# Performance work log

Hardware: AMD Instinct MI355X
Metric: run time of the kernel (lower is better)

Reference implementation:

```python
import jax, jax.numpy as jnp
import numpy as np

B, S, H, NH, HD = 2, 2048, 2048, 16, 128
E, TOPK, I = 8, 2, 2048
EPS = 1e-5
ROPE_THETA = 10000.0


def setup_inputs() -> dict:
    key = jax.random.key(0)
    ks = jax.random.split(key, 11)
    s = 0.02
    return {
        "hidden_states": jax.random.normal(ks[0], (B, S, H), jnp.float32),
        "position_ids": jnp.broadcast_to(jnp.arange(S, dtype=jnp.int32), (B, S)),
        "rms1_w": jnp.ones((H,), jnp.float32),
        "rms2_w": jnp.ones((H,), jnp.float32),
        "q_w": jax.random.normal(ks[1], (H, H), jnp.float32) * s,
        "k_w": jax.random.normal(ks[2], (H, H), jnp.float32) * s,
        "v_w": jax.random.normal(ks[3], (H, H), jnp.float32) * s,
        "o_w": jax.random.normal(ks[4], (H, H), jnp.float32) * s,
        "router_w": jax.random.normal(ks[5], (H, E), jnp.float32) * s,
        "w1": jax.random.normal(ks[6], (E, H, I), jnp.float32) * s,
        "w2": jax.random.normal(ks[7], (E, I, H), jnp.float32) * s,
        "w3": jax.random.normal(ks[8], (E, H, I), jnp.float32) * s,
    }


def rmsnorm(x, w):
    var = jnp.mean(x * x, axis=-1, keepdims=True)
    return (x * jax.lax.rsqrt(var + EPS)) * w


def rope(x, pos):
    # x: [B,S,NH,HD], pos: [B,S]
    half = HD // 2
    inv_freq = 1.0 / (ROPE_THETA ** (jnp.arange(0, half, dtype=jnp.float32) / half))
    ang = pos.astype(jnp.float32)[..., None] * inv_freq  # [B,S,half]
    cos = jnp.cos(ang)[:, :, None, :]
    sin = jnp.sin(ang)[:, :, None, :]
    x1, x2 = x[..., :half], x[..., half:]
    return jnp.concatenate([x1 * cos - x2 * sin, x2 * cos + x1 * sin], axis=-1)


def attention(x, pos, q_w, k_w, v_w, o_w):
    q = (x @ q_w).reshape(B, S, NH, HD)
    k = (x @ k_w).reshape(B, S, NH, HD)
    v = (x @ v_w).reshape(B, S, NH, HD)
    q = rope(q, pos)
    k = rope(k, pos)
    scores = jnp.einsum("bqhd,bkhd->bhqk", q, k) / np.sqrt(HD).astype(np.float32)
    causal = jnp.tril(jnp.ones((S, S), bool))
    scores = jnp.where(causal, scores, jnp.finfo(scores.dtype).min)
    probs = jax.nn.softmax(scores, axis=-1)
    ctx = jnp.einsum("bhqk,bkhd->bqhd", probs, v).reshape(B, S, H)
    return ctx @ o_w


def moe(x, router_w, w1, w2, w3):
    t = x.reshape(B * S, H)
    probs = jax.nn.softmax(t @ router_w, axis=-1)  # [T,E]
    top_v, top_i = jax.lax.top_k(probs, TOPK)
    top_v = top_v / jnp.sum(top_v, axis=-1, keepdims=True)
    T = B * S
    coeff = jnp.zeros((T, E), x.dtype).at[jnp.arange(T)[:, None], top_i].set(top_v)
    y = jnp.zeros((T, H), x.dtype)
    for e in range(E):  # fixed small expert loop
        h = jax.nn.silu(t @ w1[e]) * (t @ w3[e])
        y = y + coeff[:, e:e + 1] * (h @ w2[e])
    return y.reshape(B, S, H)


def reference(hidden_states, position_ids, rms1_w, rms2_w, q_w, k_w, v_w, o_w,
              router_w, w1, w2, w3):
    residual = hidden_states
    h = rmsnorm(hidden_states, rms1_w).astype(hidden_states.dtype)
    h = attention(h, position_ids, q_w, k_w, v_w, o_w)
    h = residual + h
    residual = h
    h = rmsnorm(h, rms2_w).astype(h.dtype)
    h = moe(h, router_w, w1, w2, w3)
    return residual + h
```

## Files before the change

kernel.cpp:

```cpp
#include <hip/hip_runtime.h>
#include <hip/hip_bf16.h>

constexpr int CB   = 2;
constexpr int CS   = 2048;
constexpr int CH   = 2048;
constexpr int CNH  = 16;
constexpr int CHD  = 128;
constexpr int CE   = 8;
constexpr int CI   = 2048;
constexpr int CT   = CB * CS;
constexpr int CQKV = 3 * CH;

typedef __attribute__((ext_vector_type(8))) short short8;
typedef __attribute__((ext_vector_type(4))) float float4v;
typedef __attribute__((ext_vector_type(4))) unsigned short ushort4v;
typedef unsigned int uint32;

__device__ __forceinline__ float bf2f(unsigned short u) {
    union { unsigned int i; float f; } x; x.i = ((unsigned int)u) << 16; return x.f;
}
__device__ __forceinline__ unsigned short f2bf(float f) {
    union { float f; unsigned int i; } x; x.f = f;
    unsigned int r = x.i + 0x7fffu + ((x.i >> 16) & 1u);
    return (unsigned short)(r >> 16);
}
__device__ __forceinline__ uint32 packpair(uint32 r0, uint32 r1) {
    return __builtin_amdgcn_perm(r1, r0, 0x07060302u);
}
__device__ __forceinline__ uint32 rnebits(float f) {
    uint32 u = __float_as_uint(f);
    return u + 0x7fffu + ((u >> 16) & 1u);
}
__device__ __forceinline__ void split2(float f0, float f1, uint32& h, uint32& l) {
    uint32 r0 = rnebits(f0), r1 = rnebits(f1);
    h = packpair(r0, r1);
    float d0 = f0 - __uint_as_float(r0 & 0xffff0000u);
    float d1 = f1 - __uint_as_float(r1 & 0xffff0000u);
    l = packpair(rnebits(d0), rnebits(d1));
}
__device__ __forceinline__ void rne16_store(const float* fv, unsigned short* dst) {
    uint32 h[8];
    #pragma unroll
    for (int p = 0; p < 8; p++) h[p] = packpair(rnebits(fv[2 * p]), rnebits(fv[2 * p + 1]));
    ((uint4*)dst)[0] = make_uint4(h[0], h[1], h[2], h[3]);
    ((uint4*)dst)[1] = make_uint4(h[4], h[5], h[6], h[7]);
}

template<int MODE>
__global__ __launch_bounds__(256) void rmsnorm_k(const float* __restrict__ x,
                                                 const float* __restrict__ w,
                                                 unsigned short* __restrict__ o1,
                                                 unsigned short* __restrict__ o2) {
    const int row = blockIdx.x;
    const float* xr = x + (size_t)row * CH;
    const int base = threadIdx.x * 8;
    float4 v0 = *(const float4*)(xr + base);
    float4 v1 = *(const float4*)(xr + base + 4);
    float ss = v0.x*v0.x + v0.y*v0.y + v0.z*v0.z + v0.w*v0.w
             + v1.x*v1.x + v1.y*v1.y + v1.z*v1.z + v1.w*v1.w;
    #pragma unroll
    for (int o = 1; o < 64; o <<= 1) ss += __shfl_xor(ss, o);
    __shared__ float ps[4];
    if ((threadIdx.x & 63) == 0) ps[threadIdx.x >> 6] = ss;
    __syncthreads();
    const float scale = rsqrtf((ps[0] + ps[1] + ps[2] + ps[3]) / (float)CH + 1e-5f);
    float4 w0 = *(const float4*)(w + base);
    float4 w1 = *(const float4*)(w + base + 4);
    float r[8] = {v0.x * scale * w0.x, v0.y * scale * w0.y, v0.z * scale * w0.z, v0.w * scale * w0.w,
                  v1.x * scale * w1.x, v1.y * scale * w1.y, v1.z * scale * w1.z, v1.w * scale * w1.w};
    if (MODE == 1) {
        rne16_store(r, o1 + (size_t)row * CH + base);
    } else {
        uint32 h[4], l[4];
        #pragma unroll
        for (int p = 0; p < 4; p++) split2(r[2 * p], r[2 * p + 1], h[p], l[p]);
        *(uint4*)(o1 + (size_t)row * CH + base) = make_uint4(h[0], h[1], h[2], h[3]);
        *(uint4*)(o2 + (size_t)row * CH + base) = make_uint4(l[0], l[1], l[2], l[3]);
    }
}

__global__ void rope_tab_k(float2* __restrict__ tab) {
    int i = blockIdx.x * 256 + threadIdx.x;
    int p = i >> 6, j = i & 63;
    double inv = pow(10000.0, -(double)j / 64.0);
    float invf = (float)inv;
    float angf = (float)p * invf;
    double da = (double)angf;
    tab[i] = make_float2((float)cos(da), (float)sin(da));
}

__global__ __launch_bounds__(256) void rope_k(unsigned short* __restrict__ qh,
                                              unsigned short* __restrict__ ql,
                                              const int* __restrict__ pos,
                                              const float2* __restrict__ tab) {
    int i = blockIdx.x * 256 + threadIdx.x;
    if (i >= CT * CNH * 64) return;
    int t = i >> 10, hj = i & 1023, hh = hj >> 6, j = hj & 63;
    float2 cs = tab[(size_t)pos[t] * 64 + j];
    unsigned short* qhp = qh + (size_t)t * CQKV + hh * CHD;
    unsigned short* qlp = ql + (size_t)t * CQKV + hh * CHD;
    #pragma unroll
    for (int s = 0; s < 2; s++) {
        unsigned short* hp = qhp + s * CH;
        unsigned short* lp = qlp + s * CH;
        float x1 = bf2f(hp[j]) + bf2f(lp[j]);
        float x2 = bf2f(hp[j + 64]) + bf2f(lp[j + 64]);
        float y1 = x1 * cs.x - x2 * cs.y;
        float y2 = x2 * cs.x + x1 * cs.y;
        uint32 r1 = rnebits(y1), r2 = rnebits(y2);
        hp[j]      = (unsigned short)(r1 >> 16);
        hp[j + 64] = (unsigned short)(r2 >> 16);
        lp[j]      = f2bf(y1 - __uint_as_float(r1 & 0xffff0000u));
        lp[j + 64] = f2bf(y2 - __uint_as_float(r2 & 0xffff0000u));
    }
}

template<int NMAT>
__global__ __launch_bounds__(256) void conv_k(const float* __restrict__ S0,
                                              const float* __restrict__ S1,
                                              unsigned short* __restrict__ D) {
    __shared__ float t[64][65];
    const int n0 = blockIdx.x * 64, k0 = blockIdx.y * 64, e = blockIdx.z;
    const size_t esrc = (size_t)e * 2048 * 2048;
    const int cc = threadIdx.x & 63, r4 = threadIdx.x >> 6;
    const int nl = threadIdx.x >> 2, q = threadIdx.x & 3;
    #pragma unroll
    for (int s = 0; s < NMAT; s++) {
        const float* S = s ? S1 : S0;
        __syncthreads();
        #pragma unroll
        for (int j = 0; j < 16; j++) {
            const int row = j * 4 + r4;
            t[cc][row] = S[esrc + (size_t)(k0 + row) * 2048 + n0 + cc];
        }
        __syncthreads();
        const int orow = (NMAT == 2) ? (2 * (n0 + nl) + s) : (n0 + nl);
        unsigned short* dp = D + (size_t)e * (NMAT * 2048) * 2048 + (size_t)orow * 2048 + k0 + q * 16;
        float fv[16];
        #pragma unroll
        for (int j = 0; j < 16; j++) fv[j] = t[nl][q * 16 + j];
        rne16_store(fv, dp);
    }
}

template<int NMAT>
__global__ __launch_bounds__(256) void convs_k(const float* __restrict__ S0,
                                               const float* __restrict__ S1,
                                               const float* __restrict__ S2,
                                               unsigned short* __restrict__ Dh,
                                               unsigned short* __restrict__ Dl) {
    __shared__ float t[64][65];
    const int n0 = blockIdx.x * 64, k0 = blockIdx.y * 64, z = blockIdx.z;
    const float* S = S0;
    if (NMAT == 3) S = (z == 0) ? S0 : ((z == 1) ? S1 : S2);
    const int cc = threadIdx.x & 63, r4 = threadIdx.x >> 6;
    #pragma unroll
    for (int j = 0; j < 16; j++) {
        const int row = j * 4 + r4;
        t[cc][row] = S[(size_t)(k0 + row) * 2048 + n0 + cc];
    }
    __syncthreads();
    const int nl = threadIdx.x >> 2, q = threadIdx.x & 3;
    float fv[16];
    #pragma unroll
    for (int j = 0; j < 16; j++) fv[j] = t[nl][q * 16 + j];
    uint32 h[8], l[8];
    #pragma unroll
    for (int p = 0; p < 8; p++) split2(fv[2 * p], fv[2 * p + 1], h[p], l[p]);
    const size_t off = (size_t)(z * 2048 + n0 + nl) * 2048 + k0 + q * 16;
    ((uint4*)(Dh + off))[0] = make_uint4(h[0], h[1], h[2], h[3]);
    ((uint4*)(Dh + off))[1] = make_uint4(h[4], h[5], h[6], h[7]);
    ((uint4*)(Dl + off))[0] = make_uint4(l[0], l[1], l[2], l[3]);
    ((uint4*)(Dl + off))[1] = make_uint4(l[4], l[5], l[6], l[7]);
}

template<int MODE>
__global__ __launch_bounds__(256) void sgemm_k(
    const unsigned short* __restrict__ Ahg, const unsigned short* __restrict__ Alg, int lda,
    const unsigned short* __restrict__ Bhg, const unsigned short* __restrict__ Blg, int K,
    unsigned short* __restrict__ Ch, unsigned short* __restrict__ Cl,
    float* __restrict__ Cf, int ldc,
    const float* __restrict__ resid, float* __restrict__ C2) {
    __shared__ unsigned short AhS[128][40], AlS[128][40], BhS[128][40], BlS[128][40];
    const int mt = blockIdx.x, nt = blockIdx.y, tid = threadIdx.x;
    const int m0 = mt * 128;
    const int srow = tid >> 1, shalf = tid & 1;
    const unsigned short* ah = Ahg + (size_t)(m0 + srow) * lda + shalf * 16;
    const unsigned short* al = Alg + (size_t)(m0 + srow) * lda + shalf * 16;
    const unsigned short* bhp = Bhg + (size_t)(nt * 128 + srow) * K + shalf * 16;
    const unsigned short* blp = Blg + (size_t)(nt * 128 + srow) * K + shalf * 16;
    const int lane = tid & 63, lr = lane & 15, lg = lane >> 4;
    const int wr = (tid >> 7) & 1, wc = (tid >> 6) & 1;

    float4v acc[4][4];
    #pragma unroll
    for (int m = 0; m < 4; m++)
        #pragma unroll
        for (int n = 0; n < 4; n++) acc[m][n] = (float4v){0.f, 0.f, 0.f, 0.f};

    short8 rah0 = *(const short8*)(ah),     rah1 = *(const short8*)(ah + 8);
    short8 ral0 = *(const short8*)(al),     ral1 = *(const short8*)(al + 8);
    short8 rbh0 = *(const short8*)(bhp),    rbh1 = *(const short8*)(bhp + 8);
    short8 rbl0 = *(const short8*)(blp),    rbl1 = *(const short8*)(blp + 8);

    for (int k0 = 0; k0 < K; k0 += 32) {
        __syncthreads();
        *(short8*)(&AhS[srow][shalf * 16])     = rah0;
        *(short8*)(&AhS[srow][shalf * 16 + 8]) = rah1;
        *(short8*)(&AlS[srow][shalf * 16])     = ral0;
        *(short8*)(&AlS[srow][shalf * 16 + 8]) = ral1;
        *(short8*)(&BhS[srow][shalf * 16])     = rbh0;
        *(short8*)(&BhS[srow][shalf * 16 + 8]) = rbh1;
        *(short8*)(&BlS[srow][shalf * 16])     = rbl0;
        *(short8*)(&BlS[srow][shalf * 16 + 8]) = rbl1;
        if (k0 + 32 < K) {
            rah0 = *(const short8*)(ah + k0 + 32);  rah1 = *(const short8*)(ah + k0 + 40);
            ral0 = *(const short8*)(al + k0 + 32);  ral1 = *(const short8*)(al + k0 + 40);
            rbh0 = *(const short8*)(bhp + k0 + 32); rbh1 = *(const short8*)(bhp + k0 + 40);
            rbl0 = *(const short8*)(blp + k0 + 32); rbl1 = *(const short8*)(blp + k0 + 40);
        }
        __syncthreads();
        short8 fah[4], fal[4], fbh[4], fbl[4];
        #pragma unroll
        for (int m = 0; m < 4; m++) {
            fah[m] = *(const short8*)(&AhS[wr * 64 + m * 16 + lr][lg * 8]);
            fal[m] = *(const short8*)(&AlS[wr * 64 + m * 16 + lr][lg * 8]);
        }
        #pragma unroll
        for (int n = 0; n < 4; n++) {
            fbh[n] = *(const short8*)(&BhS[wc * 64 + n * 16 + lr][lg * 8]);
            fbl[n] = *(const short8*)(&BlS[wc * 64 + n * 16 + lr][lg * 8]);
        }
        #pragma unroll
        for (int n = 0; n < 4; n++)
            #pragma unroll
            for (int m = 0; m < 4; m++) {
                acc[m][n] = __builtin_amdgcn_mfma_f32_16x16x32_bf16(fal[m], fbh[n], acc[m][n], 0, 0, 0);
                acc[m][n] = __builtin_amdgcn_mfma_f32_16x16x32_bf16(fah[m], fbl[n], acc[m][n], 0, 0, 0);
                acc[m][n] = __builtin_amdgcn_mfma_f32_16x16x32_bf16(fah[m], fbh[n], acc[m][n], 0, 0, 0);
            }
    }
    #pragma unroll
    for (int m = 0; m < 4; m++) {
        const int rb = wr * 64 + m * 16 + lg * 4;
        #pragma unroll
        for (int n = 0; n < 4; n++) {
            const int ccol = nt * 128 + wc * 64 + n * 16 + lr;
            #pragma unroll
            for (int r = 0; r < 4; r++) {
                const size_t idx = (size_t)(m0 + rb + r) * ldc + ccol;
                if (MODE == 1) {
                    const float v = acc[m][n][r] + resid[idx];
                    Cf[idx] = v;
                    C2[idx] = v;
                } else {
                    const float v = acc[m][n][r];
                    uint32 rr = rnebits(v);
                    Ch[idx] = (unsigned short)(rr >> 16);
                    Cl[idx] = f2bf(v - __uint_as_float(rr & 0xffff0000u));
                }
            }
        }
    }
}

template<int MODE>
__global__ __launch_bounds__(256) void gemm_k(
    const unsigned short* __restrict__ A, int lda,
    const unsigned short* __restrict__ Bt, int K, int Ne,
    void* __restrict__ Cp, int ldc,
    const int* __restrict__ cnt, const int* __restrict__ tokl,
    const float* __restrict__ gatel, const int* __restrict__ pb) {
    __shared__ unsigned short As[128][40];
    __shared__ unsigned short Bs[128][40];
    const int nt = blockIdx.x, mt = blockIdx.y, e = blockIdx.z;
    const int m0 = mt * 128;
    const int c = cnt[e];
    if (m0 >= c) return;
    const int valid = (c - m0 < 128) ? (c - m0) : 128;
    const int tid = threadIdx.x;
    const int srow = tid >> 1, shalf = tid & 1;
    size_t gr;
    if (MODE == 2) {
        const int idx = m0 + (srow < valid ? srow : valid - 1);
        gr = (size_t)tokl[e * 4096 + idx];
    } else {
        const int rr = m0 + srow;
        gr = (size_t)(pb[e] + (rr < c ? rr : c - 1));
    }
    const unsigned short* a_src = A + gr * (size_t)lda + shalf * 16;
    const unsigned short* b_src = Bt + (size_t)e * Ne * K + (size_t)(nt * 128 + srow) * K + shalf * 16;
    const int lane = tid & 63, lr = lane & 15, lg = lane >> 4;
    const int wr = (tid >> 7) & 1, wc = (tid >> 6) & 1;

    float4v acc[4][4];
    #pragma unroll
    for (int m = 0; m < 4; m++)
        #pragma unroll
        for (int n = 0; n < 4; n++) acc[m][n] = (float4v){0.f, 0.f, 0.f, 0.f};

    short8 ra0 = *(const short8*)(a_src);
    short8 ra1 = *(const short8*)(a_src + 8);
    short8 rb0 = *(const short8*)(b_src);
    short8 rb1 = *(const short8*)(b_src + 8);

    for (int k0 = 0; k0 < K; k0 += 32) {
        __syncthreads();
        *(short8*)(&As[srow][shalf * 16])     = ra0;
        *(short8*)(&As[srow][shalf * 16 + 8]) = ra1;
        *(short8*)(&Bs[srow][shalf * 16])     = rb0;
        *(short8*)(&Bs[srow][shalf * 16 + 8]) = rb1;
        if (k0 + 32 < K) {
            ra0 = *(const short8*)(a_src + k0 + 32);
            ra1 = *(const short8*)(a_src + k0 + 40);
            rb0 = *(const short8*)(b_src + k0 + 32);
            rb1 = *(const short8*)(b_src + k0 + 40);
        }
        __syncthreads();
        short8 af[4], bf[4];
        #pragma unroll
        for (int m = 0; m < 4; m++) af[m] = *(const short8*)(&As[wr * 64 + m * 16 + lr][lg * 8]);
        #pragma unroll
        for (int n = 0; n < 4; n++) bf[n] = *(const short8*)(&Bs[wc * 64 + n * 16 + lr][lg * 8]);
        #pragma unroll
        for (int n = 0; n < 4; n++)
            #pragma unroll
            for (int m = 0; m < 4; m++)
                acc[m][n] = __builtin_amdgcn_mfma_f32_16x16x32_bf16(af[m], bf[n], acc[m][n], 0, 0, 0);
    }

    #pragma unroll
    for (int m = 0; m < 4; m++) {
        const int rb = wr * 64 + m * 16 + lg * 4;
        #pragma unroll
        for (int n = 0; n < 4; n++) {
            const int col = nt * 128 + wc * 64 + n * 16 + lr;
            #pragma unroll
            for (int r = 0; r < 4; r++) {
                const int row = rb + r;
                const float v = acc[m][n][r];
                if (MODE == 2) {
                    const float other = __shfl_xor(v, 1);
                    if (!(lr & 1) && row < valid) {
                        const float g1 = v, g3 = other;
                        const float hsw = (g1 / (1.f + __expf(-g1))) * g3;
                        ((unsigned short*)Cp)[(size_t)(pb[e] + m0 + row) * ldc + (col >> 1)] = f2bf(hsw);
                    }
                } else {
                    if (row < valid) {
                        const int t = tokl[e * 4096 + m0 + row];
                        const float g = gatel[e * 4096 + m0 + row];
                        atomicAdd(((float*)Cp) + (size_t)t * ldc + col, v * g);
                    }
                }
            }
        }
    }
}

__global__ __launch_bounds__(256) void attn_k(const unsigned short* __restrict__ qh,
                                              const unsigned short* __restrict__ ql,
                                              unsigned short* __restrict__ ch,
                                              unsigned short* __restrict__ cl) {
    __shared__ unsigned short Ksh[32][136], Ksl[32][136];
    __shared__ unsigned short Vth[128][40], Vtl[128][40];
    const int qb = blockIdx.x;
    const int h  = blockIdx.y;
    const int b  = blockIdx.z;
    const int tid = threadIdx.x;
    const int wave = tid >> 6, lane = tid & 63, lr = lane & 15, lg = lane >> 4;
    const size_t tb = (size_t)b * CS;
    const int q0 = qb * 64 + wave * 16;

    short8 qfh[4], qfl[4];
    {
        const size_t off = (tb + q0 + lr) * CQKV + h * CHD;
        #pragma unroll
        for (int c = 0; c < 4; c++) {
            qfh[c] = *(const short8*)(qh + off + c * 32 + lg * 8);
            qfl[c] = *(const short8*)(ql + off + c * 32 + lg * 8);
        }
    }
    float4v o[8];
    #pragma unroll
    for (int d = 0; d < 8; d++) o[d] = (float4v){0.f, 0.f, 0.f, 0.f};
    float m = -1e30f, l = 0.f;
    const float scl = 0.08838834764831845f;
    const int ntiles = (qb * 64 + 64 + 31) >> 5;
    const int kk = tid >> 3, slot = tid & 7;
    const int vd = tid & 127, vhalf = tid >> 7;

    for (int kt = 0; kt < ntiles; ++kt) {
        const int kv0 = kt * 32;
        __syncthreads();
        {
            const size_t koff = (tb + kv0 + kk) * CQKV + CH + h * CHD + slot * 16;
            *(short8*)(&Ksh[kk][slot * 16])     = *(const short8*)(qh + koff);
            *(short8*)(&Ksh[kk][slot * 16 + 8]) = *(const short8*)(qh + koff + 8);
            *(short8*)(&Ksl[kk][slot * 16])     = *(const short8*)(ql + koff);
            *(short8*)(&Ksl[kk][slot * 16 + 8]) = *(const short8*)(ql + koff + 8);
            const size_t voff = (tb + kv0 + vhalf * 16) * CQKV + 2 * CH + h * CHD + vd;
            unsigned short th[16], tl[16];
            #pragma unroll
            for (int j = 0; j < 16; j++) {
                th[j] = qh[voff + (size_t)j * CQKV];
                tl[j] = ql[voff + (size_t)j * CQKV];
            }
            #pragma unroll
            for (int p = 0; p < 2; p++) {
                *(ushort4v*)(&Vth[vd][vhalf * 16 + p * 8])     = *(ushort4v*)(&th[p * 8]);
                *(ushort4v*)(&Vth[vd][vhalf * 16 + p * 8 + 4]) = *(ushort4v*)(&th[p * 8 + 4]);
                *(ushort4v*)(&Vtl[vd][vhalf * 16 + p * 8])     = *(ushort4v*)(&tl[p * 8]);
                *(ushort4v*)(&Vtl[vd][vhalf * 16 + p * 8 + 4]) = *(ushort4v*)(&tl[p * 8 + 4]);
            }
        }
        __syncthreads();

        float4v st0 = (float4v){0.f,0.f,0.f,0.f}, st1 = st0;
        #pragma unroll
        for (int c = 0; c < 4; c++) {
            short8 kah = *(const short8*)(&Ksh[lr][c * 32 + lg * 8]);
            short8 kal = *(const short8*)(&Ksl[lr][c * 32 + lg * 8]);
            short8 kbh = *(const short8*)(&Ksh[16 + lr][c * 32 + lg * 8]);
            short8 kbl = *(const short8*)(&Ksl[16 + lr][c * 32 + lg * 8]);
            st0 = __builtin_amdgcn_mfma_f32_16x16x32_bf16(kal, qfh[c], st0, 0, 0, 0);
            st0 = __builtin_amdgcn_mfma_f32_16x16x32_bf16(kah, qfl[c], st0, 0, 0, 0);
            st0 = __builtin_amdgcn_mfma_f32_16x16x32_bf16(kah, qfh[c], st0, 0, 0, 0);
            st1 = __builtin_amdgcn_mfma_f32_16x16x32_bf16(kbl, qfh[c], st1, 0, 0, 0);
            st1 = __builtin_amdgcn_mfma_f32_16x16x32_bf16(kbh, qfl[c], st1, 0, 0, 0);
            st1 = __builtin_amdgcn_mfma_f32_16x16x32_bf16(kbh, qfh[c], st1, 0, 0, 0);
        }
        float pv[8]; float pmax = -1e30f;
        const int qg = q0 + lr;
        #pragma unroll
        for (int f = 0; f < 2; f++) {
            #pragma unroll
            for (int r = 0; r < 4; r++) {
                const int kg = kv0 + f * 16 + lg * 4 + r;
                const float s = (kg <= qg) ? ((f ? st1[r] : st0[r]) * scl) : -1e30f;
                pv[f * 4 + r] = s;
                pmax = fmaxf(pmax, s);
            }
        }
        pmax = fmaxf(pmax, __shfl_xor(pmax, 16));
        pmax = fmaxf(pmax, __shfl_xor(pmax, 32));
        const float mnew = fmaxf(m, pmax);
        const float alpha = __expf(m - mnew);
        float sum = 0.f;
        #pragma unroll
        for (int i = 0; i < 8; i++) { const float p = __expf(pv[i] - mnew); pv[i] = p; sum += p; }
        sum += __shfl_xor(sum, 16);
        sum += __shfl_xor(sum, 32);
        l = l * alpha + sum;
        m = mnew;
        #pragma unroll
        for (int d = 0; d < 8; d++) o[d] *= alpha;
        short8 pfh, pfl;
        unsigned short* pfhp = (unsigned short*)&pfh;
        unsigned short* pflp = (unsigned short*)&pfl;
        #pragma unroll
        for (int j = 0; j < 8; j++) {
            const int srcl = (((lg & 1) * 2 + (j >> 2)) << 4) | lr;
            const float a0 = __shfl(pv[j & 3], srcl);
            const float a1 = __shfl(pv[4 + (j & 3)], srcl);
            const float sel = (lg >= 2) ? a1 : a0;
            uint32 r = rnebits(sel);
            pfhp[j] = (unsigned short)(r >> 16);
            float d = sel - __uint_as_float(r & 0xffff0000u);
            pflp[j] = (unsigned short)(rnebits(d) >> 16);
        }
        #pragma unroll
        for (int dt = 0; dt < 8; dt++) {
            short8 vh = *(const short8*)(&Vth[dt * 16 + lr][lg * 8]);
            short8 vl = *(const short8*)(&Vtl[dt * 16 + lr][lg * 8]);
            o[dt] = __builtin_amdgcn_mfma_f32_16x16x32_bf16(vl, pfh, o[dt], 0, 0, 0);
            o[dt] = __builtin_amdgcn_mfma_f32_16x16x32_bf16(vh, pfl, o[dt], 0, 0, 0);
            o[dt] = __builtin_amdgcn_mfma_f32_16x16x32_bf16(vh, pfh, o[dt], 0, 0, 0);
        }
    }
    const float inv = 1.f / l;
    const size_t coff = (tb + q0 + lr) * CH + h * CHD + lg * 4;
    #pragma unroll
    for (int dt = 0; dt < 8; dt++) {
        ushort4v wh, wl;
        #pragma unroll
        for (int r = 0; r < 4; r++) {
            const float v = o[dt][r] * inv;
            uint32 rr = rnebits(v);
            wh[r] = (unsigned short)(rr >> 16);
            wl[r] = f2bf(v - __uint_as_float(rr & 0xffff0000u));
        }
        *(ushort4v*)(ch + coff + dt * 16) = wh;
        *(ushort4v*)(cl + coff + dt * 16) = wl;
    }
}

__global__ __launch_bounds__(64) void router_k(const float* __restrict__ x,
                                               const float* __restrict__ wn,
                                               const float* __restrict__ rw,
                                               int* __restrict__ cnt, int* __restrict__ tok,
                                               float* __restrict__ gate) {
    const int t = blockIdx.x;
    const int lane = threadIdx.x;
    const float* xr = x + (size_t)t * CH;
    double ss = 0.0;
    double acc[8] = {0,0,0,0,0,0,0,0};
    for (int i = lane * 4; i < CH; i += 256) {
        float4 v = *(const float4*)(xr + i);
        float4 wv = *(const float4*)(wn + i);
        ss += (double)v.x*v.x + (double)v.y*v.y + (double)v.z*v.z + (double)v.w*v.w;
        float xs[4] = {v.x, v.y, v.z, v.w};
        float ws4[4] = {wv.x, wv.y, wv.z, wv.w};
        #pragma unroll
        for (int dd = 0; dd < 4; dd++) {
            const double xn = (double)xs[dd] * (double)ws4[dd];
            const float* rr = rw + (size_t)(i + dd) * CE;
            #pragma unroll
            for (int e2 = 0; e2 < 8; e2++) acc[e2] += xn * (double)rr[e2];
        }
    }
    #pragma unroll
    for (int o = 1; o < 64; o <<= 1) ss += __shfl_xor(ss, o);
    #pragma unroll
    for (int e2 = 0; e2 < 8; e2++) {
        #pragma unroll
        for (int o = 1; o < 64; o <<= 1) acc[e2] += __shfl_xor(acc[e2], o);
    }
    if (lane == 0) {
        const double scale = rsqrt(ss / (double)CH + 1e-5);
        int e0 = 0;
        #pragma unroll
        for (int e2 = 1; e2 < 8; e2++) if (acc[e2] > acc[e0]) e0 = e2;
        int e1 = (e0 == 0) ? 1 : 0;
        #pragma unroll
        for (int e2 = 0; e2 < 8; e2++) if (e2 != e0 && acc[e2] > acc[e1]) e1 = e2;
        const double dl = scale * (acc[e1] - acc[e0]);
        const double p1r = exp(dl);
        const float g0 = (float)(1.0 / (1.0 + p1r));
        const float g1 = (float)(p1r / (1.0 + p1r));
        int pos0 = atomicAdd(&cnt[e0], 1);
        tok[e0 * 4096 + pos0] = t; gate[e0 * 4096 + pos0] = g0;
        int pos1 = atomicAdd(&cnt[e1], 1);
        tok[e1 * 4096 + pos1] = t; gate[e1 * 4096 + pos1] = g1;
    }
}

__global__ void prefix_k(const int* __restrict__ cnt, int* __restrict__ pb) {
    if (threadIdx.x == 0 && blockIdx.x == 0) {
        int s = 0;
        for (int e = 0; e < CE; e++) { pb[e] = s; s += cnt[e]; }
    }
}

extern "C" void kernel_launch(void* const* d_in, const int* in_sizes, int n_in,
                              void* d_out, int out_size, void* d_ws, size_t ws_size,
                              hipStream_t stream) {
    (void)in_sizes; (void)n_in; (void)out_size; (void)ws_size;
    const float* hidden = (const float*)d_in[0];
    const int*   posids = (const int*)d_in[1];
    const float* rms1w  = (const float*)d_in[2];
    const float* rms2w  = (const float*)d_in[3];
    const float* qw     = (const float*)d_in[4];
    const float* kw     = (const float*)d_in[5];
    const float* vw     = (const float*)d_in[6];
    const float* ow     = (const float*)d_in[7];
    const float* rw     = (const float*)d_in[8];
    const float* w1     = (const float*)d_in[9];
    const float* w2     = (const float*)d_in[10];
    const float* w3     = (const float*)d_in[11];
    float* out = (float*)d_out;

    char* ws = (char*)d_ws;
    unsigned short* h1h = (unsigned short*)ws;
    unsigned short* h1l = (unsigned short*)(ws + 16777216);
    unsigned short* woh = (unsigned short*)ws;
    unsigned short* wol = (unsigned short*)(ws + 8388608);
    unsigned short* h2  = (unsigned short*)ws;
    int*   tok  = (int*)(ws + 16777216);
    float* gate = (float*)(ws + 16777216 + 131072);
    int*   cnt  = (int*)(ws + 16777216 + 262144);
    int*   pb   = cnt + 16;
    unsigned short* qkvh = (unsigned short*)(ws + 33554432);
    unsigned short* qkvl = (unsigned short*)(ws + 83886080);
    unsigned short* wt13 = (unsigned short*)(ws + 33554432);
    unsigned short* wt2  = (unsigned short*)(ws + 33554432);
    unsigned short* wqkvh = (unsigned short*)(ws + 134217728);
    unsigned short* wqkvl = (unsigned short*)(ws + 134217728 + 25165824);
    unsigned short* ctxh = (unsigned short*)(ws + 134217728);
    unsigned short* ctxl = (unsigned short*)(ws + 150994944);
    float*          res2 = (float*)(ws + 167772160);
    unsigned short* Hbuf = (unsigned short*)(ws + 167772160);
    float2*         rtab = (float2*)(ws + 201326592);

    rope_tab_k<<<512, 256, 0, stream>>>(rtab);
    rmsnorm_k<0><<<CT, 256, 0, stream>>>(hidden, rms1w, h1h, h1l);
    convs_k<3><<<dim3(32, 32, 3), 256, 0, stream>>>(qw, kw, vw, wqkvh, wqkvl);
    sgemm_k<0><<<dim3(32, 48), 256, 0, stream>>>(h1h, h1l, CH, wqkvh, wqkvl, CH,
                                                 qkvh, qkvl, nullptr, CQKV, nullptr, nullptr);
    rope_k<<<16384, 256, 0, stream>>>(qkvh, qkvl, posids, rtab);
    convs_k<1><<<dim3(32, 32, 1), 256, 0, stream>>>(ow, nullptr, nullptr, woh, wol);
    attn_k<<<dim3(32, CNH, CB), 256, 0, stream>>>(qkvh, qkvl, ctxh, ctxl);
    sgemm_k<1><<<dim3(32, 16), 256, 0, stream>>>(ctxh, ctxl, CH, woh, wol, CH,
                                                 nullptr, nullptr, res2, CH, hidden, out);
    rmsnorm_k<1><<<CT, 256, 0, stream>>>(res2, rms2w, h2, nullptr);
    hipMemsetAsync(cnt, 0, 8 * sizeof(int), stream);
    router_k<<<CT, 64, 0, stream>>>(res2, rms2w, rw, cnt, tok, gate);
    prefix_k<<<1, 64, 0, stream>>>(cnt, pb);
    conv_k<2><<<dim3(32, 32, CE), 256, 0, stream>>>(w1, w3, wt13);
    gemm_k<2><<<dim3(32, 32, CE), 256, 0, stream>>>(h2, CH, wt13, CH, 2 * CI, Hbuf, CI,
                                                    cnt, tok, gate, pb);
    conv_k<1><<<dim3(32, 32, CE), 256, 0, stream>>>(w2, nullptr, wt2);
    gemm_k<3><<<dim3(16, 32, CE), 256, 0, stream>>>(Hbuf, CI, wt2, CI, CH, out, CH,
                                                    cnt, tok, gate, pb);
}
```

Baseline: 1.523 ms.

## Prefetch next K/V tile into registers and remap attention blocks for XCD locality

```diff
diff --git a/kernel.cpp b/kernel.cpp
--- a/kernel.cpp
+++ b/kernel.cpp
@@ -364,9 +364,11 @@
                                               unsigned short* __restrict__ cl) {
     __shared__ unsigned short Ksh[32][136], Ksl[32][136];
     __shared__ unsigned short Vth[128][40], Vtl[128][40];
-    const int qb = blockIdx.x;
-    const int h  = blockIdx.y;
-    const int b  = blockIdx.z;
+    const int bid = blockIdx.x;
+    const int xcd = bid & 7, jj = bid >> 3;
+    const int bh  = xcd * 4 + (jj >> 5);
+    const int qb  = 31 - (jj & 31);
+    const int h   = bh & 15, b = bh >> 4;
     const int tid = threadIdx.x;
     const int wave = tid >> 6, lane = tid & 63, lr = lane & 15, lg = lane >> 4;
     const size_t tb = (size_t)b * CS;
@@ -386,32 +388,52 @@
     for (int d = 0; d < 8; d++) o[d] = (float4v){0.f, 0.f, 0.f, 0.f};
     float m = -1e30f, l = 0.f;
     const float scl = 0.08838834764831845f;
-    const int ntiles = (qb * 64 + 64 + 31) >> 5;
+    const int ntiles = 2 * (qb + 1);
     const int kk = tid >> 3, slot = tid & 7;
     const int vd = tid & 127, vhalf = tid >> 7;
 
+    short8 pkh0, pkh1, pkl0, pkl1;
+    unsigned short pth[16], ptl[16];
+    {
+        const size_t koff = (tb + kk) * CQKV + CH + h * CHD + slot * 16;
+        pkh0 = *(const short8*)(qh + koff);
+        pkh1 = *(const short8*)(qh + koff + 8);
+        pkl0 = *(const short8*)(ql + koff);
+        pkl1 = *(const short8*)(ql + koff + 8);
+        const size_t voff = (tb + vhalf * 16) * CQKV + 2 * CH + h * CHD + vd;
+        #pragma unroll
+        for (int j = 0; j < 16; j++) {
+            pth[j] = qh[voff + (size_t)j * CQKV];
+            ptl[j] = ql[voff + (size_t)j * CQKV];
+        }
+    }
+
     for (int kt = 0; kt < ntiles; ++kt) {
         const int kv0 = kt * 32;
         __syncthreads();
-        {
-            const size_t koff = (tb + kv0 + kk) * CQKV + CH + h * CHD + slot * 16;
-            *(short8*)(&Ksh[kk][slot * 16])     = *(const short8*)(qh + koff);
-            *(short8*)(&Ksh[kk][slot * 16 + 8]) = *(const short8*)(qh + koff + 8);
-            *(short8*)(&Ksl[kk][slot * 16])     = *(const short8*)(ql + koff);
-            *(short8*)(&Ksl[kk][slot * 16 + 8]) = *(const short8*)(ql + koff + 8);
-            const size_t voff = (tb + kv0 + vhalf * 16) * CQKV + 2 * CH + h * CHD + vd;
-            unsigned short th[16], tl[16];
+        *(short8*)(&Ksh[kk][slot * 16])     = pkh0;
+        *(short8*)(&Ksh[kk][slot * 16 + 8]) = pkh1;
+        *(short8*)(&Ksl[kk][slot * 16])     = pkl0;
+        *(short8*)(&Ksl[kk][slot * 16 + 8]) = pkl1;
+        #pragma unroll
+        for (int p = 0; p < 2; p++) {
+            *(ushort4v*)(&Vth[vd][vhalf * 16 + p * 8])     = *(ushort4v*)(&pth[p * 8]);
+            *(ushort4v*)(&Vth[vd][vhalf * 16 + p * 8 + 4]) = *(ushort4v*)(&pth[p * 8 + 4]);
+            *(ushort4v*)(&Vtl[vd][vhalf * 16 + p * 8])     = *(ushort4v*)(&ptl[p * 8]);
+            *(ushort4v*)(&Vtl[vd][vhalf * 16 + p * 8 + 4]) = *(ushort4v*)(&ptl[p * 8 + 4]);
+        }
+        if (kt + 1 < ntiles) {
+            const int nv0 = kv0 + 32;
+            const size_t koff = (tb + nv0 + kk) * CQKV + CH + h * CHD + slot * 16;
+            pkh0 = *(const short8*)(qh + koff);
+            pkh1 = *(const short8*)(qh + koff + 8);
+            pkl0 = *(const short8*)(ql + koff);
+            pkl1 = *(const short8*)(ql + koff + 8);
+            const size_t voff = (tb + nv0 + vhalf * 16) * CQKV + 2 * CH + h * CHD + vd;
             #pragma unroll
             for (int j = 0; j < 16; j++) {
-                th[j] = qh[voff + (size_t)j * CQKV];
-                tl[j] = ql[voff + (size_t)j * CQKV];
-            }
-            #pragma unroll
-            for (int p = 0; p < 2; p++) {
-                *(ushort4v*)(&Vth[vd][vhalf * 16 + p * 8])     = *(ushort4v*)(&th[p * 8]);
-                *(ushort4v*)(&Vth[vd][vhalf * 16 + p * 8 + 4]) = *(ushort4v*)(&th[p * 8 + 4]);
-                *(ushort4v*)(&Vtl[vd][vhalf * 16 + p * 8])     = *(ushort4v*)(&tl[p * 8]);
-                *(ushort4v*)(&Vtl[vd][vhalf * 16 + p * 8 + 4]) = *(ushort4v*)(&tl[p * 8 + 4]);
+                pth[j] = qh[voff + (size_t)j * CQKV];
+                ptl[j] = ql[voff + (size_t)j * CQKV];
             }
         }
         __syncthreads();
@@ -599,7 +621,7 @@
                                                  qkvh, qkvl, nullptr, CQKV, nullptr, nullptr);
     rope_k<<<16384, 256, 0, stream>>>(qkvh, qkvl, posids, rtab);
     convs_k<1><<<dim3(32, 32, 1), 256, 0, stream>>>(ow, nullptr, nullptr, woh, wol);
-    attn_k<<<dim3(32, CNH, CB), 256, 0, stream>>>(qkvh, qkvl, ctxh, ctxl);
+    attn_k<<<1024, 256, 0, stream>>>(qkvh, qkvl, ctxh, ctxl);
     sgemm_k<1><<<dim3(32, 16), 256, 0, stream>>>(ctxh, ctxl, CH, woh, wol, CH,
                                                  nullptr, nullptr, res2, CH, hidden, out);
     rmsnorm_k<1><<<CT, 256, 0, stream>>>(res2, rms2w, h2, nullptr);
```

After: 1.440 ms. 1.06x faster.
